# Optimization experiments

Measured on AMD Instinct MI355X. Metric: run time of the kernel, lower is better.

Reference implementation:

```python
import jax, jax.numpy as jnp
import numpy as np

B, S_DEC, S_ENC, D, H = 2, 2048, 2048, 1024, 16
HD = D // H  # 64


def setup_inputs() -> dict:
    key = jax.random.key(0)
    ks = jax.random.split(key, 12)
    s = 0.02
    return {
        "dec_hidden_state": jax.random.normal(ks[0], (B, S_DEC, D), jnp.float32),
        "enc_hidden_state": jax.random.normal(ks[1], (B, S_ENC, D), jnp.float32),
        "mask": jnp.ones((B, S_ENC, S_DEC), jnp.int32),
        "Wq": jax.random.normal(ks[2], (H, D, HD), jnp.float32) * s,
        "bq": jax.random.normal(ks[3], (H, HD), jnp.float32) * s,
        "Wk": jax.random.normal(ks[4], (H, D, HD), jnp.float32) * s,
        "bk": jax.random.normal(ks[5], (H, HD), jnp.float32) * s,
        "Wv": jax.random.normal(ks[6], (H, D, HD), jnp.float32) * s,
        "bv": jax.random.normal(ks[7], (H, HD), jnp.float32) * s,
        "Wo": jax.random.normal(ks[8], (D, D), jnp.float32) * s,
        "bo": jax.random.normal(ks[9], (D,), jnp.float32) * s,
    }


def reference(dec_hidden_state, enc_hidden_state, mask, Wq, bq, Wk, bk, Wv, bv, Wo, bo):
    # NOTE: original module swaps args: query <- enc_hidden_state, key/value <- dec_hidden_state.
    # q: [B,H,S_enc,HD], k/v: [B,H,S_dec,HD]
    q = jnp.einsum("bqd,hdk->bhqk", enc_hidden_state, Wq) + bq[None, :, None, :]
    k = jnp.einsum("bsd,hdk->bhsk", dec_hidden_state, Wk) + bk[None, :, None, :]
    v = jnp.einsum("bsd,hdk->bhsk", dec_hidden_state, Wv) + bv[None, :, None, :]
    scores = jnp.einsum("bhqk,bhsk->bhqs", q, k) / jnp.sqrt(jnp.asarray(HD, q.dtype))
    scores = jnp.where(mask[:, None, :, :] == 0, jnp.asarray(-jnp.inf, scores.dtype), scores)
    weights = jax.nn.softmax(scores, axis=-1)
    attn = jnp.einsum("bhqs,bhsk->bhqk", weights, v)  # [B,H,S_enc,HD]
    # concat heads along last dim (same order as torch.cat over head list)
    attn = jnp.transpose(attn, (0, 2, 1, 3)).reshape(B, S_ENC, D)
    return attn @ Wo + bo
```

## Files before the change

kernel.cpp:

```cpp
#include <hip/hip_runtime.h>
#include <math.h>
#include <stdint.h>


typedef unsigned short ushort_t;
typedef __attribute__((ext_vector_type(8))) short short8;
typedef __attribute__((ext_vector_type(4))) float floatx4;

__device__ __forceinline__ ushort_t f2bf(float x){
  unsigned u = __float_as_uint(x);
  u += 0x7fffu + ((u >> 16) & 1u);
  return (ushort_t)(u >> 16);
}
__device__ __forceinline__ unsigned pk2bf(float a, float b){
#if __has_builtin(__builtin_amdgcn_cvt_pk_bf16_f32)
  typedef __attribute__((ext_vector_type(2))) __bf16 bf2_t;
  bf2_t r = __builtin_amdgcn_cvt_pk_bf16_f32(a, b);
  return *(unsigned*)&r;
#else
  return (unsigned)f2bf(a) | ((unsigned)f2bf(b) << 16);
#endif
}
__device__ __forceinline__ floatx4 mfma16(short8 a, short8 b, floatx4 c){
  return __builtin_amdgcn_mfma_f32_16x16x32_bf16(a, b, c, 0, 0, 0);
}
__device__ __forceinline__ void gload16(const void* g, void* l){
  __builtin_amdgcn_global_load_lds((const __attribute__((address_space(1))) void*)g,
                                   (__attribute__((address_space(3))) void*)l, 16, 0, 0);
}

__global__ __launch_bounds__(256)
void prep_kernel(const float* __restrict__ enc, const float* __restrict__ dec,
                 const float* __restrict__ Wq, const float* __restrict__ Wk,
                 const float* __restrict__ Wv, const float* __restrict__ Wo,
                 const int* __restrict__ mask,
                 ushort_t* __restrict__ encb, ushort_t* __restrict__ decb,
                 ushort_t* __restrict__ WqT, ushort_t* __restrict__ WkT,
                 ushort_t* __restrict__ WvT, ushort_t* __restrict__ WoT,
                 unsigned long long* __restrict__ mb)
{
  __shared__ float t[64][65];
  const int bx = blockIdx.x, tid = threadIdx.x;
  if (bx < 8192){
    const float* src = (bx < 4096) ? enc : dec;
    ushort_t*    dst = (bx < 4096) ? encb : decb;
    int i = ((bx & 4095) * 256 + tid) * 4;
    const float4 v = *(const float4*)(src + i);
    unsigned long long p = (unsigned long long)f2bf(v.x)
                         | ((unsigned long long)f2bf(v.y) << 16)
                         | ((unsigned long long)f2bf(v.z) << 32)
                         | ((unsigned long long)f2bf(v.w) << 48);
    *(unsigned long long*)(dst + i) = p;
  } else if (bx < 8960){
    const int id = bx - 8192;
    const int zz = id >> 4, yy = id & 15;
    const int which = zz >> 4, head = zz & 15;
    const float* src = (which == 0) ? Wq : (which == 1) ? Wk : Wv;
    ushort_t*    dst = (which == 0) ? WqT : (which == 1) ? WkT : WvT;
    const long sb = (long)head * 65536;
    const int r0 = yy * 64;
    #pragma unroll
    for (int i = 0; i < 16; i++){
      int idx = i*256 + tid;
      int r = idx >> 6, c = idx & 63;
      t[r][c] = src[sb + (long)(r0 + r)*64 + c];
    }
    __syncthreads();
    #pragma unroll
    for (int i = 0; i < 16; i++){
      int idx = i*256 + tid;
      int cr = idx >> 6, rc = idx & 63;
      dst[sb + (long)cr*1024 + r0 + rc] = f2bf(t[rc][cr]);
    }
  } else if (bx < 9216){
    const int id = bx - 8960;
    const int r0 = (id >> 4) * 64, c0 = (id & 15) * 64;
    #pragma unroll
    for (int i = 0; i < 16; i++){
      int idx = i*256 + tid;
      int r = idx >> 6, c = idx & 63;
      t[r][c] = Wo[(long)(r0 + r)*1024 + c0 + c];
    }
    __syncthreads();
    #pragma unroll
    for (int i = 0; i < 16; i++){
      int idx = i*256 + tid;
      int cr = idx >> 6, rc = idx & 63;
      WoT[(long)(c0 + cr)*1024 + r0 + rc] = f2bf(t[rc][cr]);
    }
  } else {
    long gid = (long)(bx - 9216) * 256 + tid;
    unsigned long long bal = __ballot(mask[gid] != 0);
    if ((tid & 63) == 0) mb[gid >> 6] = bal;
  }
}

__global__ __launch_bounds__(256, 3)
void gemm_qkv_kernel(const ushort_t* __restrict__ encb, const ushort_t* __restrict__ decb,
                     const ushort_t* __restrict__ WqT, const ushort_t* __restrict__ WkT,
                     const ushort_t* __restrict__ WvT,
                     const float* __restrict__ bq, const float* __restrict__ bk,
                     const float* __restrict__ bv,
                     ushort_t* __restrict__ Qb, ushort_t* __restrict__ Kbf,
                     ushort_t* __restrict__ Vtb)
{
  __shared__ ushort_t At[2*4096];
  __shared__ ushort_t Bt[2*4096];
  const int tid = threadIdx.x;
  const int wave = tid >> 6, lane = tid & 63;
  const int quad = lane >> 4, l16 = lane & 15;
  const int z = blockIdx.z;
  const ushort_t *A, *BT; const float* bias; ushort_t* outp;
  int m0, n0; long outAdj = 0;
  float qs = 1.0f;
  if (z == 0){ A = encb; BT = WqT; bias = bq; outp = Qb;  m0 = blockIdx.x*128; n0 = blockIdx.y*128;
               qs = 0.18033688011112042f; }
  else if (z == 1){ A = decb; BT = WkT; bias = bk; outp = Kbf; m0 = blockIdx.x*128; n0 = blockIdx.y*128; }
  else {
    int id = blockIdx.x*8 + blockIdx.y;
    int vb = id >> 7, rem = id & 127;
    m0 = ((rem >> 4) & 7) * 128; n0 = (rem & 15) * 128;
    A = WvT; BT = decb + (long)vb*2097152; bias = bv; outp = Vtb; outAdj = (long)vb*2097152;
  }
  const int K = 1024;

  const int c0 = tid, c1 = 256 + tid;
  const ushort_t* gA0 = A  + (long)(m0 + (c0 >> 2))*K + (c0 & 3)*8;
  const ushort_t* gA1 = A  + (long)(m0 + (c1 >> 2))*K + (c1 & 3)*8;
  const ushort_t* gB0 = BT + (long)(n0 + (c0 >> 2))*K + (c0 & 3)*8;
  const ushort_t* gB1 = BT + (long)(n0 + (c1 >> 2))*K + (c1 & 3)*8;

  floatx4 acc[4][4];
  #pragma unroll
  for (int mt = 0; mt < 4; mt++)
    #pragma unroll
    for (int nt = 0; nt < 4; nt++)
      acc[mt][nt] = (floatx4){0.f, 0.f, 0.f, 0.f};

  {
    char* Ad = (char*)At + wave*1024;
    char* Bd = (char*)Bt + wave*1024;
    gload16(gA0, Ad); gload16(gA1, Ad + 4096);
    gload16(gB0, Bd); gload16(gB1, Bd + 4096);
    gA0 += 32; gA1 += 32; gB0 += 32; gB1 += 32;
  }

  const int moff = (wave & 1) * 64, noff = (wave >> 1) * 64;
  int cur = 0;
  for (int k0 = 0; k0 < K; k0 += 32){
    asm volatile("s_waitcnt vmcnt(0)" ::: "memory");
    __builtin_amdgcn_sched_barrier(0);
    __builtin_amdgcn_s_barrier();
    __builtin_amdgcn_sched_barrier(0);
    if (k0 + 32 < K){
      char* An = (char*)At + (cur^1)*8192 + wave*1024;
      char* Bn = (char*)Bt + (cur^1)*8192 + wave*1024;
      gload16(gA0, An); gload16(gA1, An + 4096);
      gload16(gB0, Bn); gload16(gB1, Bn + 4096);
      gA0 += 32; gA1 += 32; gB0 += 32; gB1 += 32;
    }
    short8 af[4], bfr[4];
    #pragma unroll
    for (int t = 0; t < 4; t++){
      af[t]  = *(const short8*)&At[cur*4096 + (moff + t*16 + l16)*32 + quad*8];
      bfr[t] = *(const short8*)&Bt[cur*4096 + (noff + t*16 + l16)*32 + quad*8];
    }
    #pragma unroll
    for (int mt = 0; mt < 4; mt++)
      #pragma unroll
      for (int nt = 0; nt < 4; nt++)
        acc[mt][nt] = mfma16(bfr[nt], af[mt], acc[mt][nt]);
    asm volatile("s_waitcnt lgkmcnt(0)" ::: "memory");
    __builtin_amdgcn_sched_barrier(0);
    __builtin_amdgcn_s_barrier();
    __builtin_amdgcn_sched_barrier(0);
    cur ^= 1;
  }

  #pragma unroll
  for (int mt = 0; mt < 4; mt++){
    #pragma unroll
    for (int nt = 0; nt < 4; nt++){
      floatx4 v = acc[mt][nt];
      if (z < 2){
        const int s   = m0 + moff + mt*16 + l16;
        const int ch0 = n0 + noff + nt*16 + quad*4;
        const float4 b4 = *(const float4*)&bias[ch0];
        uint2 pk;
        pk.x = pk2bf((v[0] + b4.x)*qs, (v[1] + b4.y)*qs);
        pk.y = pk2bf((v[2] + b4.z)*qs, (v[3] + b4.w)*qs);
        *(unsigned long long*)&outp[(long)s*1024 + ch0] = *(unsigned long long*)&pk;
      } else {
        const int ch = m0 + moff + mt*16 + l16;
        const int s0 = n0 + noff + nt*16 + quad*4;
        const float bb = bias[ch];
        uint2 pk;
        pk.x = pk2bf(v[0] + bb, v[1] + bb);
        pk.y = pk2bf(v[2] + bb, v[3] + bb);
        *(unsigned long long*)&outp[outAdj + (long)ch*2048 + s0] = *(unsigned long long*)&pk;
      }
    }
  }
}

__global__ __launch_bounds__(256, 2)
void gemm_o_kernel(const ushort_t* __restrict__ A, const ushort_t* __restrict__ BT,
                   const float* __restrict__ bias, float* __restrict__ outf)
{
  __shared__ ushort_t At[2*4096];
  __shared__ ushort_t Bt[2*2048];
  const int tid = threadIdx.x;
  const int wave = tid >> 6, lane = tid & 63;
  const int quad = lane >> 4, l16 = lane & 15;
  const int m0 = blockIdx.x * 128, n0 = blockIdx.y * 64;
  const int K = 1024;

  const int c0 = tid, c1 = 256 + tid;
  const ushort_t* gA0 = A  + (long)(m0 + (c0 >> 2))*K + (c0 & 3)*8;
  const ushort_t* gA1 = A  + (long)(m0 + (c1 >> 2))*K + (c1 & 3)*8;
  const ushort_t* gB0 = BT + (long)(n0 + (c0 >> 2))*K + (c0 & 3)*8;

  floatx4 acc[4][2];
  #pragma unroll
  for (int mt = 0; mt < 4; mt++)
    #pragma unroll
    for (int nt = 0; nt < 2; nt++)
      acc[mt][nt] = (floatx4){0.f, 0.f, 0.f, 0.f};

  {
    char* Ad = (char*)At + wave*1024;
    char* Bd = (char*)Bt + wave*1024;
    gload16(gA0, Ad); gload16(gA1, Ad + 4096);
    gload16(gB0, Bd);
    gA0 += 32; gA1 += 32; gB0 += 32;
  }

  const int moff = (wave & 1) * 64, noff = (wave >> 1) * 32;
  int cur = 0;
  for (int k0 = 0; k0 < K; k0 += 32){
    asm volatile("s_waitcnt vmcnt(0)" ::: "memory");
    __builtin_amdgcn_sched_barrier(0);
    __builtin_amdgcn_s_barrier();
    __builtin_amdgcn_sched_barrier(0);
    if (k0 + 32 < K){
      char* An = (char*)At + (cur^1)*8192 + wave*1024;
      char* Bn = (char*)Bt + (cur^1)*4096 + wave*1024;
      gload16(gA0, An); gload16(gA1, An + 4096);
      gload16(gB0, Bn);
      gA0 += 32; gA1 += 32; gB0 += 32;
    }
    short8 af[4], bfr[2];
    #pragma unroll
    for (int t = 0; t < 4; t++)
      af[t]  = *(const short8*)&At[cur*4096 + (moff + t*16 + l16)*32 + quad*8];
    #pragma unroll
    for (int t = 0; t < 2; t++)
      bfr[t] = *(const short8*)&Bt[cur*2048 + (noff + t*16 + l16)*32 + quad*8];
    #pragma unroll
    for (int mt = 0; mt < 4; mt++)
      #pragma unroll
      for (int nt = 0; nt < 2; nt++)
        acc[mt][nt] = mfma16(bfr[nt], af[mt], acc[mt][nt]);
    asm volatile("s_waitcnt lgkmcnt(0)" ::: "memory");
    __builtin_amdgcn_sched_barrier(0);
    __builtin_amdgcn_s_barrier();
    __builtin_amdgcn_sched_barrier(0);
    cur ^= 1;
  }

  #pragma unroll
  for (int mt = 0; mt < 4; mt++){
    #pragma unroll
    for (int nt = 0; nt < 2; nt++){
      const int s   = m0 + moff + mt*16 + l16;
      const int ch0 = n0 + noff + nt*16 + quad*4;
      const float4 b4 = *(const float4*)&bias[ch0];
      float4 o;
      o.x = acc[mt][nt][0] + b4.x;
      o.y = acc[mt][nt][1] + b4.y;
      o.z = acc[mt][nt][2] + b4.z;
      o.w = acc[mt][nt][3] + b4.w;
      *(float4*)&outf[(long)s*1024 + ch0] = o;
    }
  }
}

#define SM_PB(zA_, zB_, wv_, lsum_, pb_)                              \
  {                                                                   \
    float p0 = __builtin_amdgcn_exp2f((zA_)[0]);                      \
    float p1 = __builtin_amdgcn_exp2f((zA_)[1]);                      \
    float p2 = __builtin_amdgcn_exp2f((zA_)[2]);                      \
    float p3 = __builtin_amdgcn_exp2f((zA_)[3]);                      \
    float p4 = __builtin_amdgcn_exp2f((zB_)[0]);                      \
    float p5 = __builtin_amdgcn_exp2f((zB_)[1]);                      \
    float p6 = __builtin_amdgcn_exp2f((zB_)[2]);                      \
    float p7 = __builtin_amdgcn_exp2f((zB_)[3]);                      \
    if (__builtin_expect(!uni, 0)){                                   \
      const int sh_ = quad*8;                                         \
      p0 = (((wv_) >> (sh_+0)) & 1u) ? p0 : 0.f;                      \
      p1 = (((wv_) >> (sh_+1)) & 1u) ? p1 : 0.f;                      \
      p2 = (((wv_) >> (sh_+2)) & 1u) ? p2 : 0.f;                      \
      p3 = (((wv_) >> (sh_+3)) & 1u) ? p3 : 0.f;                      \
      p4 = (((wv_) >> (sh_+4)) & 1u) ? p4 : 0.f;                      \
      p5 = (((wv_) >> (sh_+5)) & 1u) ? p5 : 0.f;                      \
      p6 = (((wv_) >> (sh_+6)) & 1u) ? p6 : 0.f;                      \
      p7 = (((wv_) >> (sh_+7)) & 1u) ? p7 : 0.f;                      \
    }                                                                 \
    lsum_ += ((p0 + p1) + (p2 + p3)) + ((p4 + p5) + (p6 + p7));       \
    unsigned pk0_ = pk2bf(p0, p1);                                    \
    unsigned pk1_ = pk2bf(p2, p3);                                    \
    unsigned pk2_ = pk2bf(p4, p5);                                    \
    unsigned pk3_ = pk2bf(p6, p7);                                    \
    unsigned tmp_[4] = {pk0_, pk1_, pk2_, pk3_};                      \
    __builtin_memcpy(&(pb_), tmp_, 16);                               \
  }

__global__ __launch_bounds__(512, 4)
void flash_attn_kernel(const ushort_t* __restrict__ Qp, const ushort_t* __restrict__ Kp,
                       const ushort_t* __restrict__ Vt, const unsigned* __restrict__ mb,
                       ushort_t* __restrict__ aout)
{
  __shared__ __align__(16) unsigned char smem_raw[65536];
  ushort_t* KBs = (ushort_t*)smem_raw;
  ushort_t* VBs = KBs + 16384;
  float* mO = (float*)smem_raw;
  float* mL = (float*)(smem_raw + 32768);

  const int tid = threadIdx.x, wave = tid >> 6, lane = tid & 63;
  const int quad = lane >> 4, l16 = lane & 15;
  const int shalf = wave >> 2, w = wave & 3;
  const int bh = blockIdx.x, qt = blockIdx.y;
  const int b = bh >> 4, h = bh & 15;

  const ushort_t* VB = Vt + (long)bh*131072;
  const int q0 = qt*128 + w*32;

  const int l8 = lane >> 3, cl = lane & 7;
  const int r0 = w*16 + l8;
  const int sr0 = (r0 & 35) | ((r0 & 4) << 1) | ((r0 & 16) >> 2);
  const int cg = cl ^ l8;
  const ushort_t* kp0 = Kp + ((long)b*2048 + shalf*1024 + sr0)*1024 + h*64 + cg*8;
  const ushort_t* kp1 = kp0 + 16384;
  const ushort_t* vp0 = VB + (long)r0*2048 + shalf*1024 + cg*8;
  const ushort_t* vp1 = vp0 + 16384;
  const int kdo = shalf*16384 + w*2048;
  const int vdo = 32768 + shalf*16384 + w*2048;

  {
    char* kd = (char*)smem_raw + kdo;
    gload16(kp0, kd); gload16(kp1, kd + 1024);
    char* vd = (char*)smem_raw + vdo;
    gload16(vp0, vd); gload16(vp1, vd + 1024);
    kp0 += 65536; kp1 += 65536; vp0 += 64; vp1 += 64;
  }

  short8 qfA0, qfA1, qfB0, qfB1;
  {
    const long qrowA = ((long)b*2048 + q0 + l16)*1024 + h*64;
    qfA0 = *(const short8*)&Qp[qrowA +      quad*8];
    qfA1 = *(const short8*)&Qp[qrowA + 32 + quad*8];
    const long qrowB = qrowA + 16*1024;
    qfB0 = *(const short8*)&Qp[qrowB +      quad*8];
    qfB1 = *(const short8*)&Qp[qrowB + 32 + quad*8];
  }

  floatx4 accA[4], accB[4];
  #pragma unroll
  for (int ht = 0; ht < 4; ht++){
    accA[ht] = (floatx4){0.f,0.f,0.f,0.f};
    accB[ht] = (floatx4){0.f,0.f,0.f,0.f};
  }
  float lsA = 0.f, lsB = 0.f;

  const uint2* mb2 = (const uint2*)mb;
  const long mbase = (long)b*2048 + q0;
  const int sw8 = l16 & 7;
  const int kc0 = (quad ^ sw8) * 8;
  const int kc1 = kc0 ^ 32;

  int cur = 0;
  for (int st = 0; st < 16; st++){
    const uint2 mwA = mb2[(mbase +      l16)*32 + shalf*16 + st];
    const uint2 mwB = mb2[(mbase + 16 + l16)*32 + shalf*16 + st];
    __builtin_amdgcn_sched_barrier(0);
    if (st < 15){
      char* kd = (char*)smem_raw + kdo + (cur^1)*8192;
      gload16(kp0, kd); gload16(kp1, kd + 1024);
      char* vd = (char*)smem_raw + vdo + (cur^1)*8192;
      gload16(vp0, vd); gload16(vp1, vd + 1024);
      kp0 += 65536; kp1 += 65536; vp0 += 64; vp1 += 64;
      asm volatile("s_waitcnt vmcnt(6)" ::: "memory");
    } else {
      asm volatile("s_waitcnt vmcnt(0)" ::: "memory");
    }
    __builtin_amdgcn_s_barrier();
    __builtin_amdgcn_sched_barrier(0);

    const ushort_t* Kt = KBs + shalf*8192 + cur*4096;
    const ushort_t* Vp = VBs + shalf*8192 + cur*4096;
    const bool uni = __all((mwA.x & mwA.y & mwB.x & mwB.y) == 0xFFFFFFFFu);

    #pragma unroll
    for (int c = 0; c < 2; c++){
      const int rA = (c*2    )*16 + l16;
      const int rB = (c*2 + 1)*16 + l16;
      short8 kA0 = *(const short8*)&Kt[rA*64 + kc0];
      short8 kA1 = *(const short8*)&Kt[rA*64 + kc1];
      short8 kB0 = *(const short8*)&Kt[rB*64 + kc0];
      short8 kB1 = *(const short8*)&Kt[rB*64 + kc1];

      floatx4 zA = (floatx4){0.f,0.f,0.f,0.f};
      zA = mfma16(kA0, qfA0, zA);
      zA = mfma16(kA1, qfA1, zA);
      floatx4 zB = (floatx4){0.f,0.f,0.f,0.f};
      zB = mfma16(kB0, qfA0, zB);
      zB = mfma16(kB1, qfA1, zB);
      const unsigned wvA = c ? mwA.y : mwA.x;
      short8 pbA;
      SM_PB(zA, zB, wvA, lsA, pbA);

      zA = (floatx4){0.f,0.f,0.f,0.f};
      zA = mfma16(kA0, qfB0, zA);
      zA = mfma16(kA1, qfB1, zA);
      zB = (floatx4){0.f,0.f,0.f,0.f};
      zB = mfma16(kB0, qfB0, zB);
      zB = mfma16(kB1, qfB1, zB);
      const unsigned wvB = c ? mwB.y : mwB.x;
      short8 pbB;
      SM_PB(zA, zB, wvB, lsB, pbB);

      const int vcs = ((c*4 + quad) ^ sw8) * 8;
      #pragma unroll
      for (int ht = 0; ht < 4; ht++){
        const short8 vf = *(const short8*)&Vp[(ht*16 + l16)*64 + vcs];
        accA[ht] = mfma16(vf, pbA, accA[ht]);
        accB[ht] = mfma16(vf, pbB, accB[ht]);
      }
    }

    asm volatile("s_waitcnt lgkmcnt(0)" ::: "memory");
    __builtin_amdgcn_sched_barrier(0);
    __builtin_amdgcn_s_barrier();
    __builtin_amdgcn_sched_barrier(0);
    cur ^= 1;
  }

  lsA += __shfl_xor(lsA, 16);
  lsA += __shfl_xor(lsA, 32);
  lsB += __shfl_xor(lsB, 16);
  lsB += __shfl_xor(lsB, 32);

  __syncthreads();
  if (shalf == 1){
    #pragma unroll
    for (int ht = 0; ht < 4; ht++){
      *(floatx4*)&mO[((((w*2 + 0)*4 + ht)*64) + lane)*4] = accA[ht];
      *(floatx4*)&mO[((((w*2 + 1)*4 + ht)*64) + lane)*4] = accB[ht];
    }
    mL[(w*2 + 0)*64 + lane] = lsA;
    mL[(w*2 + 1)*64 + lane] = lsB;
  }
  __syncthreads();
  if (shalf == 0){
    const float invA = 1.0f / (lsA + mL[(w*2 + 0)*64 + lane]);
    const float invB = 1.0f / (lsB + mL[(w*2 + 1)*64 + lane]);
    const long rowoA = ((long)b*2048 + q0 + l16)*1024 + h*64;
    const long rowoB = rowoA + 16*1024;
    #pragma unroll
    for (int ht = 0; ht < 4; ht++){
      const floatx4 oA = *(const floatx4*)&mO[((((w*2 + 0)*4 + ht)*64) + lane)*4];
      uint2 pkA;
      pkA.x = pk2bf((accA[ht][0] + oA[0])*invA, (accA[ht][1] + oA[1])*invA);
      pkA.y = pk2bf((accA[ht][2] + oA[2])*invA, (accA[ht][3] + oA[3])*invA);
      *(unsigned long long*)&aout[rowoA + ht*16 + quad*4] = *(unsigned long long*)&pkA;
      const floatx4 oB = *(const floatx4*)&mO[((((w*2 + 1)*4 + ht)*64) + lane)*4];
      uint2 pkB;
      pkB.x = pk2bf((accB[ht][0] + oB[0])*invB, (accB[ht][1] + oB[1])*invB);
      pkB.y = pk2bf((accB[ht][2] + oB[2])*invB, (accB[ht][3] + oB[3])*invB);
      *(unsigned long long*)&aout[rowoB + ht*16 + quad*4] = *(unsigned long long*)&pkB;
    }
  }
}

extern "C" void kernel_launch(void* const* d_in, const int* in_sizes, int n_in,
                              void* d_out, int out_size, void* d_ws, size_t ws_size,
                              hipStream_t stream) {
  const float* dec  = (const float*)d_in[0];
  const float* enc  = (const float*)d_in[1];
  const int*   mask = (const int*)d_in[2];
  const float* Wq   = (const float*)d_in[3];
  const float* bq   = (const float*)d_in[4];
  const float* Wk   = (const float*)d_in[5];
  const float* bk   = (const float*)d_in[6];
  const float* Wv   = (const float*)d_in[7];
  const float* bv   = (const float*)d_in[8];
  const float* Wo   = (const float*)d_in[9];
  const float* bo   = (const float*)d_in[10];
  float* out = (float*)d_out;

  ushort_t* ws   = (ushort_t*)d_ws;
  ushort_t* encb = ws;
  ushort_t* decb = encb + 4194304;
  ushort_t* Qb   = decb + 4194304;
  ushort_t* Kbf  = Qb   + 4194304;
  ushort_t* Vtb  = Kbf  + 4194304;
  ushort_t* WqT  = Vtb  + 4194304;
  ushort_t* WkT  = WqT  + 1048576;
  ushort_t* WvT  = WkT  + 1048576;
  ushort_t* WoT  = WvT  + 1048576;
  unsigned* Mb   = (unsigned*)(WoT + 1048576);

  prep_kernel<<<41984, 256, 0, stream>>>(enc, dec, Wq, Wk, Wv, Wo, mask,
                                         encb, decb, WqT, WkT, WvT, WoT,
                                         (unsigned long long*)Mb);
  gemm_qkv_kernel<<<dim3(32,8,3), 256, 0, stream>>>(encb, decb, WqT, WkT, WvT,
                                                    bq, bk, bv, Qb, Kbf, Vtb);
  flash_attn_kernel<<<dim3(32,16,1), 512, 0, stream>>>(Qb, Kbf, Vtb, Mb, encb);
  gemm_o_kernel<<<dim3(32,16,1), 256, 0, stream>>>(encb, WoT, bo, out);
}
```

Baseline: 244.6 us.

## Give each wave a private K/V staging buffer and drop block barriers

Before, all waves cooperatively loaded shared double-buffered K/V tiles and synchronised with block-wide barriers on every step. Now each wave stages its own 32-key K tile and V slice into a private LDS region, reloads the next tile right after pulling fragments into registers, and runs 32 steps with no s_barrier. MFMA sections are wrapped in s_setprio. This removes cross-wave synchronisation stalls, but each wave now loads K/V itself, so the four waves sharing a key half repeat the same global loads, and each step waits on vmcnt(0) with little prefetch overlap.

```diff
diff --git a/kernel.cpp b/kernel.cpp
--- a/kernel.cpp
+++ b/kernel.cpp
@@ -315,44 +315,50 @@
     __builtin_memcpy(&(pb_), tmp_, 16);                               \
   }
 
+#define STAGE_KV()  do {                       \
+    gload16(kp,         kd);                   \
+    gload16(kp + 16384, kd + 1024);            \
+    gload16(kp + 4096,  kd + 2048);            \
+    gload16(kp + 20480, kd + 3072);            \
+    gload16(vp,         vd);                   \
+    gload16(vp + 32768, vd + 1024);            \
+    gload16(vp + 65536, vd + 2048);            \
+    gload16(vp + 98304, vd + 3072);            \
+  } while(0)
+
 __global__ __launch_bounds__(512, 4)
 void flash_attn_kernel(const ushort_t* __restrict__ Qp, const ushort_t* __restrict__ Kp,
                        const ushort_t* __restrict__ Vt, const unsigned* __restrict__ mb,
                        ushort_t* __restrict__ aout)
 {
   __shared__ __align__(16) unsigned char smem_raw[65536];
-  ushort_t* KBs = (ushort_t*)smem_raw;
-  ushort_t* VBs = KBs + 16384;
   float* mO = (float*)smem_raw;
   float* mL = (float*)(smem_raw + 32768);
 
   const int tid = threadIdx.x, wave = tid >> 6, lane = tid & 63;
   const int quad = lane >> 4, l16 = lane & 15;
-  const int shalf = wave >> 2, w = wave & 3;
+  const int shalf = wave >> 2, qp = wave & 3;
   const int bh = blockIdx.x, qt = blockIdx.y;
   const int b = bh >> 4, h = bh & 15;
 
   const ushort_t* VB = Vt + (long)bh*131072;
-  const int q0 = qt*128 + w*32;
-
-  const int l8 = lane >> 3, cl = lane & 7;
-  const int r0 = w*16 + l8;
-  const int sr0 = (r0 & 35) | ((r0 & 4) << 1) | ((r0 & 16) >> 2);
-  const int cg = cl ^ l8;
-  const ushort_t* kp0 = Kp + ((long)b*2048 + shalf*1024 + sr0)*1024 + h*64 + cg*8;
-  const ushort_t* kp1 = kp0 + 16384;
-  const ushort_t* vp0 = VB + (long)r0*2048 + shalf*1024 + cg*8;
-  const ushort_t* vp1 = vp0 + 16384;
-  const int kdo = shalf*16384 + w*2048;
-  const int vdo = 32768 + shalf*16384 + w*2048;
-
-  {
-    char* kd = (char*)smem_raw + kdo;
-    gload16(kp0, kd); gload16(kp1, kd + 1024);
-    char* vd = (char*)smem_raw + vdo;
-    gload16(vp0, vd); gload16(vp1, vd + 1024);
-    kp0 += 65536; kp1 += 65536; vp0 += 64; vp1 += 64;
-  }
+  const int q0 = qt*128 + qp*32;
+
+  char* kd = (char*)smem_raw + wave*4096;
+  char* vd = (char*)smem_raw + 32768 + wave*4096;
+  const ushort_t* Kt = (const ushort_t*)kd;
+  const ushort_t* Vp = (const ushort_t*)vd;
+
+  const int l8 = lane >> 3, cl8 = lane & 7;
+  const int s0 = (l8 & 3) | ((l8 & 4) << 1);
+  const int kcg = cl8 ^ l8;
+  const ushort_t* kp = Kp + ((long)b*2048 + shalf*1024 + s0)*1024 + h*64 + kcg*8;
+  const int vr0 = lane >> 2;
+  const int vcg = (lane & 3) ^ ((lane >> 2) & 3) ^ ((lane >> 4) & 3);
+  const ushort_t* vp = VB + (long)vr0*2048 + shalf*1024 + vcg*8;
+
+  STAGE_KV();
+  kp += 32768; vp += 32;
 
   short8 qfA0, qfA1, qfB0, qfB1;
   {
@@ -372,77 +378,56 @@
   }
   float lsA = 0.f, lsB = 0.f;
 
-  const uint2* mb2 = (const uint2*)mb;
-  const long mbase = (long)b*2048 + q0;
-  const int sw8 = l16 & 7;
-  const int kc0 = (quad ^ sw8) * 8;
+  const unsigned* mpa = mb + ((long)b*2048 + q0 +      l16)*64 + shalf*32;
+  const unsigned* mpb = mb + ((long)b*2048 + q0 + 16 + l16)*64 + shalf*32;
+  const int kc0 = (quad ^ (l16 & 7)) * 8;
   const int kc1 = kc0 ^ 32;
-
-  int cur = 0;
-  for (int st = 0; st < 16; st++){
-    const uint2 mwA = mb2[(mbase +      l16)*32 + shalf*16 + st];
-    const uint2 mwB = mb2[(mbase + 16 + l16)*32 + shalf*16 + st];
-    __builtin_amdgcn_sched_barrier(0);
-    if (st < 15){
-      char* kd = (char*)smem_raw + kdo + (cur^1)*8192;
-      gload16(kp0, kd); gload16(kp1, kd + 1024);
-      char* vd = (char*)smem_raw + vdo + (cur^1)*8192;
-      gload16(vp0, vd); gload16(vp1, vd + 1024);
-      kp0 += 65536; kp1 += 65536; vp0 += 64; vp1 += 64;
-      asm volatile("s_waitcnt vmcnt(6)" ::: "memory");
-    } else {
-      asm volatile("s_waitcnt vmcnt(0)" ::: "memory");
-    }
-    __builtin_amdgcn_s_barrier();
-    __builtin_amdgcn_sched_barrier(0);
-
-    const ushort_t* Kt = KBs + shalf*8192 + cur*4096;
-    const ushort_t* Vp = VBs + shalf*8192 + cur*4096;
-    const bool uni = __all((mwA.x & mwA.y & mwB.x & mwB.y) == 0xFFFFFFFFu);
-
-    #pragma unroll
-    for (int c = 0; c < 2; c++){
-      const int rA = (c*2    )*16 + l16;
-      const int rB = (c*2 + 1)*16 + l16;
-      short8 kA0 = *(const short8*)&Kt[rA*64 + kc0];
-      short8 kA1 = *(const short8*)&Kt[rA*64 + kc1];
-      short8 kB0 = *(const short8*)&Kt[rB*64 + kc0];
-      short8 kB1 = *(const short8*)&Kt[rB*64 + kc1];
-
-      floatx4 zA = (floatx4){0.f,0.f,0.f,0.f};
-      zA = mfma16(kA0, qfA0, zA);
-      zA = mfma16(kA1, qfA1, zA);
-      floatx4 zB = (floatx4){0.f,0.f,0.f,0.f};
-      zB = mfma16(kB0, qfA0, zB);
-      zB = mfma16(kB1, qfA1, zB);
-      const unsigned wvA = c ? mwA.y : mwA.x;
-      short8 pbA;
-      SM_PB(zA, zB, wvA, lsA, pbA);
-
-      zA = (floatx4){0.f,0.f,0.f,0.f};
-      zA = mfma16(kA0, qfB0, zA);
-      zA = mfma16(kA1, qfB1, zA);
-      zB = (floatx4){0.f,0.f,0.f,0.f};
-      zB = mfma16(kB0, qfB0, zB);
-      zB = mfma16(kB1, qfB1, zB);
-      const unsigned wvB = c ? mwB.y : mwB.x;
-      short8 pbB;
-      SM_PB(zA, zB, wvB, lsB, pbB);
-
-      const int vcs = ((c*4 + quad) ^ sw8) * 8;
-      #pragma unroll
-      for (int ht = 0; ht < 4; ht++){
-        const short8 vf = *(const short8*)&Vp[(ht*16 + l16)*64 + vcs];
-        accA[ht] = mfma16(vf, pbA, accA[ht]);
-        accB[ht] = mfma16(vf, pbB, accB[ht]);
-      }
-    }
-
+  const int vcs = (quad ^ (l16 & 3) ^ ((l16 >> 2) & 3)) * 8;
+
+  for (int st = 0; st < 32; ++st){
+    asm volatile("s_waitcnt vmcnt(0)" ::: "memory");
+    __builtin_amdgcn_sched_barrier(0);
+    const unsigned mwA = mpa[st];
+    const unsigned mwB = mpb[st];
+    short8 kA0 = *(const short8*)&Kt[(     l16)*64 + kc0];
+    short8 kA1 = *(const short8*)&Kt[(     l16)*64 + kc1];
+    short8 kB0 = *(const short8*)&Kt[(16 + l16)*64 + kc0];
+    short8 kB1 = *(const short8*)&Kt[(16 + l16)*64 + kc1];
+    short8 vf0 = *(const short8*)&Vp[(     l16)*32 + vcs];
+    short8 vf1 = *(const short8*)&Vp[(16 + l16)*32 + vcs];
+    short8 vf2 = *(const short8*)&Vp[(32 + l16)*32 + vcs];
+    short8 vf3 = *(const short8*)&Vp[(48 + l16)*32 + vcs];
     asm volatile("s_waitcnt lgkmcnt(0)" ::: "memory");
     __builtin_amdgcn_sched_barrier(0);
-    __builtin_amdgcn_s_barrier();
-    __builtin_amdgcn_sched_barrier(0);
-    cur ^= 1;
+    if (st < 31){
+      STAGE_KV();
+      kp += 32768; vp += 32;
+    }
+    __builtin_amdgcn_sched_barrier(0);
+
+    const bool uni = __all((mwA & mwB) == 0xFFFFFFFFu);
+    __builtin_amdgcn_s_setprio(1);
+    floatx4 zA = (floatx4){0.f,0.f,0.f,0.f};
+    zA = mfma16(kA0, qfA0, zA);
+    zA = mfma16(kA1, qfA1, zA);
+    floatx4 zB = (floatx4){0.f,0.f,0.f,0.f};
+    zB = mfma16(kB0, qfA0, zB);
+    zB = mfma16(kB1, qfA1, zB);
+    short8 pbA;
+    SM_PB(zA, zB, mwA, lsA, pbA);
+    zA = (floatx4){0.f,0.f,0.f,0.f};
+    zA = mfma16(kA0, qfB0, zA);
+    zA = mfma16(kA1, qfB1, zA);
+    zB = (floatx4){0.f,0.f,0.f,0.f};
+    zB = mfma16(kB0, qfB0, zB);
+    zB = mfma16(kB1, qfB1, zB);
+    short8 pbB;
+    SM_PB(zA, zB, mwB, lsB, pbB);
+    accA[0] = mfma16(vf0, pbA, accA[0]);  accB[0] = mfma16(vf0, pbB, accB[0]);
+    accA[1] = mfma16(vf1, pbA, accA[1]);  accB[1] = mfma16(vf1, pbB, accB[1]);
+    accA[2] = mfma16(vf2, pbA, accA[2]);  accB[2] = mfma16(vf2, pbB, accB[2]);
+    accA[3] = mfma16(vf3, pbA, accA[3]);  accB[3] = mfma16(vf3, pbB, accB[3]);
+    __builtin_amdgcn_s_setprio(0);
   }
 
   lsA += __shfl_xor(lsA, 16);
@@ -454,26 +439,26 @@
   if (shalf == 1){
     #pragma unroll
     for (int ht = 0; ht < 4; ht++){
-      *(floatx4*)&mO[((((w*2 + 0)*4 + ht)*64) + lane)*4] = accA[ht];
-      *(floatx4*)&mO[((((w*2 + 1)*4 + ht)*64) + lane)*4] = accB[ht];
-    }
-    mL[(w*2 + 0)*64 + lane] = lsA;
-    mL[(w*2 + 1)*64 + lane] = lsB;
+      *(floatx4*)&mO[((((qp*2 + 0)*4 + ht)*64) + lane)*4] = accA[ht];
+      *(floatx4*)&mO[((((qp*2 + 1)*4 + ht)*64) + lane)*4] = accB[ht];
+    }
+    mL[(qp*2 + 0)*64 + lane] = lsA;
+    mL[(qp*2 + 1)*64 + lane] = lsB;
   }
   __syncthreads();
   if (shalf == 0){
-    const float invA = 1.0f / (lsA + mL[(w*2 + 0)*64 + lane]);
-    const float invB = 1.0f / (lsB + mL[(w*2 + 1)*64 + lane]);
+    const float invA = 1.0f / (lsA + mL[(qp*2 + 0)*64 + lane]);
+    const float invB = 1.0f / (lsB + mL[(qp*2 + 1)*64 + lane]);
     const long rowoA = ((long)b*2048 + q0 + l16)*1024 + h*64;
     const long rowoB = rowoA + 16*1024;
     #pragma unroll
     for (int ht = 0; ht < 4; ht++){
-      const floatx4 oA = *(const floatx4*)&mO[((((w*2 + 0)*4 + ht)*64) + lane)*4];
+      const floatx4 oA = *(const floatx4*)&mO[((((qp*2 + 0)*4 + ht)*64) + lane)*4];
       uint2 pkA;
       pkA.x = pk2bf((accA[ht][0] + oA[0])*invA, (accA[ht][1] + oA[1])*invA);
       pkA.y = pk2bf((accA[ht][2] + oA[2])*invA, (accA[ht][3] + oA[3])*invA);
       *(unsigned long long*)&aout[rowoA + ht*16 + quad*4] = *(unsigned long long*)&pkA;
-      const floatx4 oB = *(const floatx4*)&mO[((((w*2 + 1)*4 + ht)*64) + lane)*4];
+      const floatx4 oB = *(const floatx4*)&mO[((((qp*2 + 1)*4 + ht)*64) + lane)*4];
       uint2 pkB;
       pkB.x = pk2bf((accB[ht][0] + oB[0])*invB, (accB[ht][1] + oB[1])*invB);
       pkB.y = pk2bf((accB[ht][2] + oB[2])*invB, (accB[ht][3] + oB[3])*invB);
@@ -481,6 +466,7 @@
     }
   }
 }
+#undef STAGE_KV
 
 extern "C" void kernel_launch(void* const* d_in, const int* in_sizes, int n_in,
                               void* d_out, int out_size, void* d_ws, size_t ws_size,
```

Result: slower. 263.9 us (+7.9%).
